# Optimization experiments

Hardware: AMD Instinct MI355X
Metric: run time of the kernel (lower is better)

## Reference

```python
import jax, jax.numpy as jnp
import numpy as np

KH, KW = 3, 3
PAD, STRIDE = 1, 1
KD = 3  # depth kernel extent; extended with one zero slice -> 4 indices


def _unfold(x, pad, stride):
    # x: (B, C, H, W) -> (B, C, KH*KW, oH, oW), patches ordered row-major like F.unfold
    B, C, H, W = x.shape
    xp = jnp.pad(x, ((0, 0), (0, 0), (pad, pad), (pad, pad)))
    oH = (H + 2 * pad - KH) // stride + 1
    oW = (W + 2 * pad - KW) // stride + 1
    pats = [xp[:, :, i:i + (oH - 1) * stride + 1:stride, j:j + (oW - 1) * stride + 1:stride]
            for i in range(KH) for j in range(KW)]
    return jnp.stack(pats, axis=2)


def setup_inputs() -> dict:
    key = jax.random.key(0)
    k1, k2, k3 = jax.random.split(key, 3)
    features = jax.random.normal(k1, (4, 16, 512, 512), dtype=jnp.float32)
    depth = jax.random.randint(k2, (4, 512, 512), 0, 8, dtype=jnp.int32)
    weight = jax.random.normal(k3, (32, 16, 3, 3, 3), dtype=jnp.float32) * 0.05
    return {"features": features, "depth": depth, "weight": weight}


def reference(features, depth, weight):
    oC, iC = weight.shape[0], weight.shape[1]
    # unfolded input patches: (B, iC, 9, oH, oW)
    patches = _unfold(features, PAD, STRIDE)
    # unfolded depth: (B, 9, oH, oW); padding fills with depth 0 (matches F.unfold)
    dpat = _unfold(depth[:, None, :, :].astype(jnp.int32), PAD, STRIDE)[:, 0]
    center = dpat[:, KH * KW // 2][:, None]  # (B, 1, oH, oW)
    diff = dpat - center
    # diff < -1 or diff >= 1 -> select appended zero slice (index 3); else diff+1
    idx = jnp.where((diff < -1) | (diff >= 1), 3, diff + 1)  # (B, 9, oH, oW) in [0, 3]
    onehot = jax.nn.one_hot(idx, KD + 1, dtype=features.dtype)  # (B, 9, oH, oW, 4)
    # extended weight with zero depth-slice: (oC, iC, 4, 9)
    ext_w = jnp.concatenate([weight, jnp.zeros_like(weight[:, :, :1])], axis=2)
    ext_w = ext_w.reshape(oC, iC, KD + 1, KH * KW)
    # per-pixel depth-gated 3x3x3 conv (bias is never added in the original op)
    out = jnp.einsum('oidk,bkhwd,bikhw->bohw', ext_w, onehot, patches)
    return out
```

## Files before the change

### kernel.cpp

```cpp
#include <hip/hip_runtime.h>
#include <hip/hip_bf16.h>


#define IC 16
#define OC 32
#define Hh 512
#define Ww 512
#define HW (Hh * Ww)
#define TW 256
#define TR 4
#define PXS 20
#define SENT (1 << 20)

typedef __attribute__((ext_vector_type(8))) short short8;
typedef __attribute__((ext_vector_type(4))) float float4v;
typedef __attribute__((ext_vector_type(2))) unsigned int uint2v;

__device__ __forceinline__ unsigned short f2bf(float x) {
    unsigned u = __float_as_uint(x);
    unsigned r = u + 0x7FFFu + ((u >> 16) & 1u);
    return (unsigned short)(r >> 16);
}

__device__ __forceinline__ unsigned packbf(float a, float b) {
    union { __hip_bfloat162 h2; unsigned u; } cv;
    cv.h2 = __float22bfloat162_rn(make_float2(a, b));
    return cv.u;
}

__global__ void prep_weights(const float* __restrict__ wgt,
                             unsigned short* __restrict__ wsA) {
    int e = blockIdx.x * 256 + threadIdx.x;
    if (e >= 9 * 2 * 64 * 8) return;
    int j    = e & 7;
    int lane = (e >> 3) & 63;
    int mt   = (e >> 9) & 1;
    int c    = e >> 10;
    int oc = mt * 16 + (lane & 15);
    int kk = ((lane >> 4) << 3) + j;
    wsA[e] = f2bf(wgt[oc * 432 + (kk >> 1) * 27 + (kk & 1) * 9 + c]);
}

__global__ __launch_bounds__(512, 2) void depconv_fused(
    const float* __restrict__ feat,
    const int*   __restrict__ depth,
    const unsigned short* __restrict__ wsA,
    float*       __restrict__ out)
{
    __shared__ unsigned short ftile[TR + 2][TW + 2][PXS];
    __shared__ int            dtile[TR + 2][TW + 2];

    const int tid = threadIdx.x;

    const int bid = blockIdx.x;
    const int wg  = (bid & 7) * (1024 / 8) + (bid >> 3);

    const int b      = wg >> 8;
    const int rowblk = (wg >> 1) & 127;
    const int colblk = wg & 1;
    const int h0     = rowblk * TR;
    const int wstart = colblk * TW;

    {
        const int h8 = tid >> 8;
        const int xl = tid & 255;
        const int x  = wstart - 1 + xl;
        const bool xin = (unsigned)x < (unsigned)Ww;
        const int xc = x < 0 ? 0 : (x > Ww - 1 ? Ww - 1 : x);
        const int xt  = wstart - 1 + 256 + xl;
        const bool xtin = (unsigned)xt < (unsigned)Ww;
        const int xct = xt > Ww - 1 ? Ww - 1 : xt;
        const float* fb  = feat + (size_t)(b * IC + 8 * h8) * HW;
        const int*   dbp = depth + (b << 18);
#pragma unroll
        for (int r = 0; r < 6; ++r) {
            const int y = h0 - 1 + r;
            const bool yin = (unsigned)y < (unsigned)Hh;
            const int yc = y < 0 ? 0 : (y > Hh - 1 ? Hh - 1 : y);
            const float* fpl = fb + (size_t)yc * Ww;
            if (h8 == 0) {
                dtile[r][xl] = (yin & xin) ? dbp[yc * Ww + xc] : SENT;
                if (xl < 2)
                    dtile[r][256 + xl] = (yin & xtin) ? dbp[yc * Ww + xct] : SENT;
            }
            unsigned pk[4];
#pragma unroll
            for (int i = 0; i < 4; ++i)
                pk[i] = packbf(fpl[(size_t)(2 * i) * HW + xc],
                               fpl[(size_t)(2 * i + 1) * HW + xc]);
            unsigned short* wp = &ftile[r][xl][h8 * 8];
            *(uint2v*)wp       = (uint2v){pk[0], pk[1]};
            *(uint2v*)(wp + 4) = (uint2v){pk[2], pk[3]};
            if (xl < 2) {
                unsigned qk[4];
#pragma unroll
                for (int i = 0; i < 4; ++i)
                    qk[i] = packbf(fpl[(size_t)(2 * i) * HW + xct],
                                   fpl[(size_t)(2 * i + 1) * HW + xct]);
                unsigned short* wq = &ftile[r][256 + xl][h8 * 8];
                *(uint2v*)wq       = (uint2v){qk[0], qk[1]};
                *(uint2v*)(wq + 4) = (uint2v){qk[2], qk[3]};
            }
        }
    }

    const int lane = tid & 63;
    short8 wfrag[9][2];
    {
        const short8* ap = (const short8*)wsA;
#pragma unroll
        for (int c = 0; c < 9; ++c) {
            wfrag[c][0] = ap[(c * 2 + 0) * 64 + lane];
            wfrag[c][1] = ap[(c * 2 + 1) * 64 + lane];
        }
    }
    __syncthreads();

    const int wv   = tid >> 6;
    const int g    = lane >> 4;
    const int n    = lane & 15;
    const int rr   = wv >> 1;
    const int h    = h0 + rr;
    const int xoff = (wv & 1) * 128;

    const int q   = lane >> 4;
    const int oc0 = lane & 15;
    float* opb0 = out + ((size_t)(b * OC + oc0) << 18) + (size_t)h * Ww;

    for (int it = 0; it < 8; ++it) {
        const int xb = xoff + it * 16 + n;
        const int dc = dtile[rr + 1][xb + 1];

        float4v acc0 = {0.f, 0.f, 0.f, 0.f};
        float4v acc1 = {0.f, 0.f, 0.f, 0.f};

#pragma unroll
        for (int t = 0; t < 9; ++t) {
            const int kh = t / 3, kw = t % 3;
            unsigned mm;
            if (t == 4) {
                mm = 0xffff0000u;
            } else {
                const int diff = dtile[rr + kh][xb + kw] - dc;
                mm = (diff == 0) ? 0xffff0000u : ((diff == -1) ? 0x0000ffffu : 0u);
            }
            const uint2v pr = *(const uint2v*)(&ftile[rr + kh][xb + kw][g << 2]);
            union { short8 s; unsigned u[4]; } bf;
            bf.u[0] = __builtin_amdgcn_perm(0u, pr.x, 0x01000100u) & mm;
            bf.u[1] = __builtin_amdgcn_perm(0u, pr.x, 0x03020302u) & mm;
            bf.u[2] = __builtin_amdgcn_perm(0u, pr.y, 0x01000100u) & mm;
            bf.u[3] = __builtin_amdgcn_perm(0u, pr.y, 0x03020302u) & mm;

            acc0 = __builtin_amdgcn_mfma_f32_16x16x32_bf16(bf.s, wfrag[t][0], acc0, 0, 0, 0);
            acc1 = __builtin_amdgcn_mfma_f32_16x16x32_bf16(bf.s, wfrag[t][1], acc1, 0, 0, 0);
        }

        const int w16 = wstart + xoff + it * 16;
        float* op = opb0 + (w16 + 4 * q);
        *(float4v*)op                       = acc0;
        *(float4v*)(op + (size_t)16 * HW)   = acc1;
    }
}

extern "C" void kernel_launch(void* const* d_in, const int* in_sizes, int n_in,
                              void* d_out, int out_size, void* d_ws, size_t ws_size,
                              hipStream_t stream) {
    const float* feat  = (const float*)d_in[0];
    const int*   depth = (const int*)d_in[1];
    const float* wgt   = (const float*)d_in[2];
    float* out = (float*)d_out;

    unsigned short* wsA = (unsigned short*)d_ws;

    prep_weights<<<36, 256, 0, stream>>>(wgt, wsA);
    depconv_fused<<<1024, 512, 0, stream>>>(feat, depth, wsA, out);
}
```

Measured before the change: 238.4 us.

## Make blocks persistent over four tiles with double-buffered register prefetch

Each block now handles four consecutive tiles instead of one, with 256 blocks launched in place of 1024. It double-buffers the LDS tiles and prefetches the next tile's features and depth into registers while the current tile is computed. The goal is to hide global load latency behind MFMA work and to load the weight fragments once per block rather than once per tile. In exchange, register pressure rises (48 prefetch floats), occupancy drops to one block per CU, and the LDS footprint doubles. The grid is also smaller, about one block per CU, which may underfill the device.

```diff
diff --git a/kernel.cpp b/kernel.cpp
--- a/kernel.cpp
+++ b/kernel.cpp
@@ -11,6 +11,7 @@
 #define TR 4
 #define PXS 20
 #define SENT (1 << 20)
+#define NT 4
 
 typedef __attribute__((ext_vector_type(8))) short short8;
 typedef __attribute__((ext_vector_type(4))) float float4v;
@@ -41,124 +42,153 @@
     wsA[e] = f2bf(wgt[oc * 432 + (kk >> 1) * 27 + (kk & 1) * 9 + c]);
 }
 
-__global__ __launch_bounds__(512, 2) void depconv_fused(
+__global__ __launch_bounds__(512, 1) void depconv_fused(
     const float* __restrict__ feat,
     const int*   __restrict__ depth,
     const unsigned short* __restrict__ wsA,
     float*       __restrict__ out)
 {
-    __shared__ unsigned short ftile[TR + 2][TW + 2][PXS];
-    __shared__ int            dtile[TR + 2][TW + 2];
+    __shared__ unsigned short ftile[2][6][TW + 2][PXS];
+    __shared__ int            dtile[2][6][TW + 2];
 
     const int tid = threadIdx.x;
-
     const int bid = blockIdx.x;
-    const int wg  = (bid & 7) * (1024 / 8) + (bid >> 3);
-
-    const int b      = wg >> 8;
-    const int rowblk = (wg >> 1) & 127;
-    const int colblk = wg & 1;
-    const int h0     = rowblk * TR;
-    const int wstart = colblk * TW;
-
+    const int wg = (bid & 7) * 32 + (bid >> 3);
+    const int t0 = wg * NT;
+
+    const int h8 = tid >> 8;
+    const int xl = tid & 255;
+
+    const int lane = tid & 63;
+    const int wv   = tid >> 6;
+    const int g    = lane >> 4;
+    const int n    = lane & 15;
+    const int rr   = wv >> 1;
+    const int xoff = (wv & 1) * 128;
+    const int q    = lane >> 4;
+    const int oc0  = lane & 15;
+
+    short8 wfrag[9][2];
     {
-        const int h8 = tid >> 8;
-        const int xl = tid & 255;
-        const int x  = wstart - 1 + xl;
+        const short8* ap = (const short8*)wsA;
+#pragma unroll
+        for (int c = 0; c < 9; ++c) {
+            wfrag[c][0] = ap[(c * 2 + 0) * 64 + lane];
+            wfrag[c][1] = ap[(c * 2 + 1) * 64 + lane];
+        }
+    }
+
+    float pf[6][8];
+    int   pd[6];
+
+    auto issue = [&](int tt) {
+        const int b      = tt >> 8;
+        const int h0     = ((tt >> 1) & 127) * TR;
+        const int wstart = (tt & 1) * TW;
+        const int x   = wstart - 1 + xl;
         const bool xin = (unsigned)x < (unsigned)Ww;
-        const int xc = x < 0 ? 0 : (x > Ww - 1 ? Ww - 1 : x);
-        const int xt  = wstart - 1 + 256 + xl;
-        const bool xtin = (unsigned)xt < (unsigned)Ww;
-        const int xct = xt > Ww - 1 ? Ww - 1 : xt;
-        const float* fb  = feat + (size_t)(b * IC + 8 * h8) * HW;
-        const int*   dbp = depth + (b << 18);
+        const int xc  = x < 0 ? 0 : (x > Ww - 1 ? Ww - 1 : x);
+        const float* fb  = feat + (size_t)(b * IC + 8 * h8) * HW + xc;
+        const int*   dbp = depth + (b << 18) + xc;
 #pragma unroll
         for (int r = 0; r < 6; ++r) {
             const int y = h0 - 1 + r;
             const bool yin = (unsigned)y < (unsigned)Hh;
             const int yc = y < 0 ? 0 : (y > Hh - 1 ? Hh - 1 : y);
             const float* fpl = fb + (size_t)yc * Ww;
-            if (h8 == 0) {
-                dtile[r][xl] = (yin & xin) ? dbp[yc * Ww + xc] : SENT;
-                if (xl < 2)
-                    dtile[r][256 + xl] = (yin & xtin) ? dbp[yc * Ww + xct] : SENT;
+            if (h8 == 0) pd[r] = (yin & xin) ? dbp[yc * Ww] : SENT;
+#pragma unroll
+            for (int i = 0; i < 8; ++i)
+                pf[r][i] = fpl[(size_t)i * HW];
+        }
+    };
+
+    auto write_tile = [&](int p, int tt) {
+        const int b      = tt >> 8;
+        const int h0     = ((tt >> 1) & 127) * TR;
+        const int wstart = (tt & 1) * TW;
+#pragma unroll
+        for (int r = 0; r < 6; ++r) {
+            if (h8 == 0) dtile[p][r][xl] = pd[r];
+            unsigned short* wp = &ftile[p][r][xl][h8 * 8];
+            *(uint2v*)wp       = (uint2v){packbf(pf[r][0], pf[r][1]),
+                                          packbf(pf[r][2], pf[r][3])};
+            *(uint2v*)(wp + 4) = (uint2v){packbf(pf[r][4], pf[r][5]),
+                                          packbf(pf[r][6], pf[r][7])};
+        }
+        if (xl < 2) {
+            const int xt = wstart - 1 + 256 + xl;
+            const bool xtin = (unsigned)xt < (unsigned)Ww;
+            const int xct = xt > Ww - 1 ? Ww - 1 : xt;
+            const float* fb  = feat + (size_t)(b * IC + 8 * h8) * HW + xct;
+            const int*   dbp = depth + (b << 18) + xct;
+#pragma unroll
+            for (int r = 0; r < 6; ++r) {
+                const int y = h0 - 1 + r;
+                const bool yin = (unsigned)y < (unsigned)Hh;
+                const int yc = y < 0 ? 0 : (y > Hh - 1 ? Hh - 1 : y);
+                const float* fpl = fb + (size_t)yc * Ww;
+                if (h8 == 0)
+                    dtile[p][r][256 + xl] = (yin & xtin) ? dbp[yc * Ww] : SENT;
+                unsigned short* wq = &ftile[p][r][256 + xl][h8 * 8];
+                *(uint2v*)wq       = (uint2v){packbf(fpl[0],              fpl[(size_t)1 * HW]),
+                                              packbf(fpl[(size_t)2 * HW], fpl[(size_t)3 * HW])};
+                *(uint2v*)(wq + 4) = (uint2v){packbf(fpl[(size_t)4 * HW], fpl[(size_t)5 * HW]),
+                                              packbf(fpl[(size_t)6 * HW], fpl[(size_t)7 * HW])};
             }
-            unsigned pk[4];
-#pragma unroll
-            for (int i = 0; i < 4; ++i)
-                pk[i] = packbf(fpl[(size_t)(2 * i) * HW + xc],
-                               fpl[(size_t)(2 * i + 1) * HW + xc]);
-            unsigned short* wp = &ftile[r][xl][h8 * 8];
-            *(uint2v*)wp       = (uint2v){pk[0], pk[1]};
-            *(uint2v*)(wp + 4) = (uint2v){pk[2], pk[3]};
-            if (xl < 2) {
-                unsigned qk[4];
-#pragma unroll
-                for (int i = 0; i < 4; ++i)
-                    qk[i] = packbf(fpl[(size_t)(2 * i) * HW + xct],
-                                   fpl[(size_t)(2 * i + 1) * HW + xct]);
-                unsigned short* wq = &ftile[r][256 + xl][h8 * 8];
-                *(uint2v*)wq       = (uint2v){qk[0], qk[1]};
-                *(uint2v*)(wq + 4) = (uint2v){qk[2], qk[3]};
+        }
+    };
+
+    auto compute = [&](int p, int tt) {
+        const int b      = tt >> 8;
+        const int h0     = ((tt >> 1) & 127) * TR;
+        const int wstart = (tt & 1) * TW;
+        const int h = h0 + rr;
+        float* opb0 = out + ((size_t)(b * OC + oc0) << 18) + (size_t)h * Ww;
+        for (int it = 0; it < 8; ++it) {
+            const int xb = xoff + it * 16 + n;
+            const int dc = dtile[p][rr + 1][xb + 1];
+            float4v acc0 = {0.f, 0.f, 0.f, 0.f};
+            float4v acc1 = {0.f, 0.f, 0.f, 0.f};
+#pragma unroll
+            for (int t = 0; t < 9; ++t) {
+                const int kh = t / 3, kw = t % 3;
+                unsigned mm;
+                if (t == 4) {
+                    mm = 0xffff0000u;
+                } else {
+                    const int diff = dtile[p][rr + kh][xb + kw] - dc;
+                    mm = (diff == 0) ? 0xffff0000u : ((diff == -1) ? 0x0000ffffu : 0u);
+                }
+                const uint2v pr = *(const uint2v*)(&ftile[p][rr + kh][xb + kw][g << 2]);
+                union { short8 s; unsigned u[4]; } bf;
+                bf.u[0] = __builtin_amdgcn_perm(0u, pr.x, 0x01000100u) & mm;
+                bf.u[1] = __builtin_amdgcn_perm(0u, pr.x, 0x03020302u) & mm;
+                bf.u[2] = __builtin_amdgcn_perm(0u, pr.y, 0x01000100u) & mm;
+                bf.u[3] = __builtin_amdgcn_perm(0u, pr.y, 0x03020302u) & mm;
+
+                acc0 = __builtin_amdgcn_mfma_f32_16x16x32_bf16(bf.s, wfrag[t][0], acc0, 0, 0, 0);
+                acc1 = __builtin_amdgcn_mfma_f32_16x16x32_bf16(bf.s, wfrag[t][1], acc1, 0, 0, 0);
             }
-        }
-    }
-
-    const int lane = tid & 63;
-    short8 wfrag[9][2];
-    {
-        const short8* ap = (const short8*)wsA;
-#pragma unroll
-        for (int c = 0; c < 9; ++c) {
-            wfrag[c][0] = ap[(c * 2 + 0) * 64 + lane];
-            wfrag[c][1] = ap[(c * 2 + 1) * 64 + lane];
-        }
-    }
+            const int w16 = wstart + xoff + it * 16;
+            float* op = opb0 + (w16 + 4 * q);
+            *(float4v*)op                     = acc0;
+            *(float4v*)(op + (size_t)16 * HW) = acc1;
+        }
+    };
+
+    issue(t0);
+    write_tile(0, t0);
     __syncthreads();
-
-    const int wv   = tid >> 6;
-    const int g    = lane >> 4;
-    const int n    = lane & 15;
-    const int rr   = wv >> 1;
-    const int h    = h0 + rr;
-    const int xoff = (wv & 1) * 128;
-
-    const int q   = lane >> 4;
-    const int oc0 = lane & 15;
-    float* opb0 = out + ((size_t)(b * OC + oc0) << 18) + (size_t)h * Ww;
-
-    for (int it = 0; it < 8; ++it) {
-        const int xb = xoff + it * 16 + n;
-        const int dc = dtile[rr + 1][xb + 1];
-
-        float4v acc0 = {0.f, 0.f, 0.f, 0.f};
-        float4v acc1 = {0.f, 0.f, 0.f, 0.f};
-
-#pragma unroll
-        for (int t = 0; t < 9; ++t) {
-            const int kh = t / 3, kw = t % 3;
-            unsigned mm;
-            if (t == 4) {
-                mm = 0xffff0000u;
-            } else {
-                const int diff = dtile[rr + kh][xb + kw] - dc;
-                mm = (diff == 0) ? 0xffff0000u : ((diff == -1) ? 0x0000ffffu : 0u);
-            }
-            const uint2v pr = *(const uint2v*)(&ftile[rr + kh][xb + kw][g << 2]);
-            union { short8 s; unsigned u[4]; } bf;
-            bf.u[0] = __builtin_amdgcn_perm(0u, pr.x, 0x01000100u) & mm;
-            bf.u[1] = __builtin_amdgcn_perm(0u, pr.x, 0x03020302u) & mm;
-            bf.u[2] = __builtin_amdgcn_perm(0u, pr.y, 0x01000100u) & mm;
-            bf.u[3] = __builtin_amdgcn_perm(0u, pr.y, 0x03020302u) & mm;
-
-            acc0 = __builtin_amdgcn_mfma_f32_16x16x32_bf16(bf.s, wfrag[t][0], acc0, 0, 0, 0);
-            acc1 = __builtin_amdgcn_mfma_f32_16x16x32_bf16(bf.s, wfrag[t][1], acc1, 0, 0, 0);
-        }
-
-        const int w16 = wstart + xoff + it * 16;
-        float* op = opb0 + (w16 + 4 * q);
-        *(float4v*)op                       = acc0;
-        *(float4v*)(op + (size_t)16 * HW)   = acc1;
+#pragma unroll 1
+    for (int i = 0; i < NT; ++i) {
+        const int p = i & 1;
+        if (i + 1 < NT) issue(t0 + i + 1);
+        compute(p, t0 + i);
+        if (i + 1 < NT) {
+            write_tile(p ^ 1, t0 + i + 1);
+            __syncthreads();
+        }
     }
 }
 
@@ -173,5 +203,5 @@
     unsigned short* wsA = (unsigned short*)d_ws;
 
     prep_weights<<<36, 256, 0, stream>>>(wgt, wsA);
-    depconv_fused<<<1024, 512, 0, stream>>>(feat, depth, wsA, out);
-}
+    depconv_fused<<<256, 512, 0, stream>>>(feat, depth, wsA, out);
+}
```

Measured after the change: 216.7 us. 9.1% less time.
